# Kernel tuning notes

Hardware: AMD Instinct MI355X
Metric: run time of the kernel (lower is better)

## Reference

```python
import jax, jax.numpy as jnp
import numpy as np

B, S, D_MODEL, D_K, D_V, H = 2, 2048, 1024, 1024, 1024, 16


def setup_inputs() -> dict:
    key = jax.random.key(0)
    ks = jax.random.split(key, 12)
    s = 0.02
    inp = {
        "queries": jax.random.normal(ks[0], (B, S, D_MODEL), jnp.float32),
        "keys": jax.random.normal(ks[1], (B, S, D_MODEL), jnp.float32),
        "values": jax.random.normal(ks[2], (B, S, D_MODEL), jnp.float32),
        # causal mask: 1 where attention is disallowed (added as -1e9*mask)
        "mask": jnp.triu(jnp.ones((1, 1, S, S), jnp.float32), k=1),
        "Wq": jax.random.normal(ks[3], (D_MODEL, D_K), jnp.float32) * s,
        "bq": jnp.zeros((D_K,), jnp.float32),
        "Wk": jax.random.normal(ks[4], (D_MODEL, D_K), jnp.float32) * s,
        "bk": jnp.zeros((D_K,), jnp.float32),
        "Wv": jax.random.normal(ks[5], (D_MODEL, D_V), jnp.float32) * s,
        "bv": jnp.zeros((D_V,), jnp.float32),
        "Wo": jax.random.normal(ks[6], (D_K, D_MODEL), jnp.float32) * s,
        "bo": jnp.zeros((D_MODEL,), jnp.float32),
    }
    return inp


def _split_heads(x):  # [B,S,D] -> [B,H,S,D/H]
    b, s, d = x.shape
    return x.reshape(b, s, H, d // H).transpose(0, 2, 1, 3)


def reference(queries, keys, values, mask, Wq, bq, Wk, bk, Wv, bv, Wo, bo):
    q = _split_heads(queries @ Wq + bq)   # [B,H,S,hd]
    k = _split_heads(keys @ Wk + bk)
    v = _split_heads(values @ Wv + bv)
    # NOTE: original scales by sqrt(full d_k), not per-head dim (faithful quirk)
    scores = jnp.einsum("bhqd,bhkd->bhqk", q, k) / jnp.sqrt(jnp.float32(D_K))
    scores = scores + (-1e9) * mask
    w = jax.nn.softmax(scores, axis=-1)
    out = jnp.einsum("bhqk,bhkd->bhqd", w, v)        # [B,H,S,hd]
    out = out.transpose(0, 2, 1, 3).reshape(q.shape[0], q.shape[2], D_K)
    return out @ Wo + bo
```

## Files before the change

kernel.cpp:

```cpp
#include <hip/hip_runtime.h>
#include <hip/hip_bf16.h>
#include <cstdint>

typedef __bf16 bf16;
typedef __bf16 bf16x2 __attribute__((ext_vector_type(2)));
typedef __bf16 bf16x4 __attribute__((ext_vector_type(4)));
typedef __bf16 bf16x8 __attribute__((ext_vector_type(8)));
typedef float f32x4 __attribute__((ext_vector_type(4)));
typedef float f32x16 __attribute__((ext_vector_type(16)));
typedef unsigned int u32;

#define B_ 2
#define S_ 2048
#define DM 1024
#define H_ 16
#define HD 64

__device__ __forceinline__ void gload_lds16(const bf16* g, bf16* l) {
  __builtin_amdgcn_global_load_lds((const __attribute__((address_space(1))) void*)g,
                                   (__attribute__((address_space(3))) void*)l,
                                   16, 0, 0);
}

__device__ __forceinline__ u32 cvt_pk_bf16(float lo, float hi) {
  u32 r;
  asm("v_cvt_pk_bf16_f32 %0, %1, %2" : "=v"(r) : "v"(lo), "v"(hi));
  return r;
}

__global__ __launch_bounds__(256) void convert_k(const float* __restrict__ s0,
                                                 const float* __restrict__ s1,
                                                 const float* __restrict__ s2,
                                                 bf16* __restrict__ d0,
                                                 bf16* __restrict__ d1,
                                                 bf16* __restrict__ d2) {
  const float* s = (blockIdx.z == 0) ? s0 : (blockIdx.z == 1) ? s1 : s2;
  bf16* d = (blockIdx.z == 0) ? d0 : (blockIdx.z == 1) ? d1 : d2;
  const size_t i = ((size_t)blockIdx.x * 256 + threadIdx.x) * 8;
  f32x4 a = *(const f32x4*)(s + i);
  f32x4 b = *(const f32x4*)(s + i + 4);
  bf16x8 o;
#pragma unroll
  for (int j = 0; j < 4; j++) { o[j] = (bf16)a[j]; o[j + 4] = (bf16)b[j]; }
  *(bf16x8*)(d + i) = o;
}

__global__ __launch_bounds__(256) void transposeW_k(
    const float* __restrict__ w0, const float* __restrict__ w1,
    const float* __restrict__ w2, const float* __restrict__ w3,
    bf16* __restrict__ t0, bf16* __restrict__ t1,
    bf16* __restrict__ t2, bf16* __restrict__ t3) {
  const float* src = (blockIdx.z == 0) ? w0 : (blockIdx.z == 1) ? w1
                     : (blockIdx.z == 2) ? w2 : w3;
  bf16* dst = (blockIdx.z == 0) ? t0 : (blockIdx.z == 1) ? t1
              : (blockIdx.z == 2) ? t2 : t3;
  __shared__ float tile[32][33];
  const int tx = threadIdx.x, ty = threadIdx.y;
  const int x0 = blockIdx.x * 32, y0 = blockIdx.y * 32;
#pragma unroll
  for (int r = 0; r < 4; r++)
    tile[ty + r * 8][tx] = src[(size_t)(y0 + ty + r * 8) * DM + x0 + tx];
  __syncthreads();
#pragma unroll
  for (int r = 0; r < 4; r++)
    dst[(size_t)(x0 + ty + r * 8) * DM + y0 + tx] = (bf16)tile[tx][ty + r * 8];
}

struct GArgs { const void* A; const bf16* Bt; const float* bias; void* C; };
struct GArgs3 { GArgs g[3]; };

__global__ __launch_bounds__(512, 1) void gemm128_k(GArgs3 args, int M, int N,
                                                    int K) {
  __shared__ __align__(16) bf16 SA_[73728];
  bf16* const SB_ = SA_ + 24576;

  const int nwg = gridDim.x;
  const int id = blockIdx.x;
  const int wgid = (id & 7) * (nwg >> 3) + (id >> 3);
  const int z = wgid >> 7;
  const int rem = wgid & 127;
  const int tx = rem >> 5, ty = rem & 31;
  const GArgs ga = args.g[z];
  const int m0 = ty * 128, n0 = tx * 256;

  const int tid = threadIdx.x;
  const int lane = tid & 63, w = tid >> 6;
  const int l15 = lane & 15, q = lane >> 4;
  const int wr = w >> 2, wc = w & 3;

  const bf16* gA[2];
  const bf16* gB[4];
  int dA[2], dB[4];
#pragma unroll
  for (int i = 0; i < 2; i++) {
    const int ci = i * 512 + w * 64 + lane;
    const int row = ci >> 3, sc = (ci & 7) ^ (row & 7);
    gA[i] = (const bf16*)ga.A + (size_t)(m0 + row) * K + sc * 8;
    dA[i] = (i * 512 + w * 64) * 8;
  }
#pragma unroll
  for (int i = 0; i < 4; i++) {
    const int ci = i * 512 + w * 64 + lane;
    const int row = ci >> 3, sc = (ci & 7) ^ (row & 7);
    gB[i] = ga.Bt + (size_t)(n0 + row) * K + sc * 8;
    dB[i] = (i * 512 + w * 64) * 8;
  }

  const int cA0 = (q ^ (l15 & 7)) * 8;
  const int cA1 = ((4 + q) ^ (l15 & 7)) * 8;

  f32x4 acc[4][4] = {};

  const int NT = K >> 6;

#pragma unroll
  for (int tt = 0; tt < 2; tt++) {
    bf16* Ab = SA_ + tt * 8192;
    bf16* Bb = SB_ + tt * 16384;
    const int k0 = tt * 64;
    gload_lds16(gA[0] + k0, Ab + dA[0]);
    gload_lds16(gA[1] + k0, Ab + dA[1]);
#pragma unroll
    for (int i = 0; i < 4; i++) gload_lds16(gB[i] + k0, Bb + dB[i]);
  }
  asm volatile("s_waitcnt vmcnt(6)" ::: "memory");
  __builtin_amdgcn_s_barrier();

  for (int t = 0; t < NT; ++t) {
    const int rb = t % 3;
    const int wb = (t + 2) % 3;
    const int kpre = ((t + 2 < NT) ? t + 2 : NT - 1) << 6;
    {
      bf16* Ab = SA_ + wb * 8192;
      bf16* Bb = SB_ + wb * 16384;
      gload_lds16(gA[0] + kpre, Ab + dA[0]);
      gload_lds16(gA[1] + kpre, Ab + dA[1]);
#pragma unroll
      for (int i = 0; i < 4; i++) gload_lds16(gB[i] + kpre, Bb + dB[i]);
    }

    const bf16* Ab = SA_ + rb * 8192;
    const bf16* Bb = SB_ + rb * 16384;
    bf16x8 a[4][2], b[4][2];
#pragma unroll
    for (int mt = 0; mt < 4; mt++) {
      const int ro = (wr * 64 + mt * 16 + l15) * 64;
      a[mt][0] = *(const bf16x8*)(Ab + ro + cA0);
      a[mt][1] = *(const bf16x8*)(Ab + ro + cA1);
    }
#pragma unroll
    for (int nt = 0; nt < 4; nt++) {
      const int ro = (wc * 64 + nt * 16 + l15) * 64;
      b[nt][0] = *(const bf16x8*)(Bb + ro + cA0);
      b[nt][1] = *(const bf16x8*)(Bb + ro + cA1);
    }

    __builtin_amdgcn_s_setprio(1);
#pragma unroll
    for (int mt = 0; mt < 4; mt++)
#pragma unroll
      for (int nt = 0; nt < 4; nt++)
#pragma unroll
        for (int kk = 0; kk < 2; kk++)
          acc[mt][nt] = __builtin_amdgcn_mfma_f32_16x16x32_bf16(
              a[mt][kk], b[nt][kk], acc[mt][nt], 0, 0, 0);
    __builtin_amdgcn_s_setprio(0);

    asm volatile("s_waitcnt vmcnt(6)" ::: "memory");
    __builtin_amdgcn_s_barrier();
  }

  asm volatile("s_waitcnt vmcnt(0)" ::: "memory");
  __builtin_amdgcn_s_barrier();

  bf16* Ws = SA_ + w * 4352;
#pragma unroll
  for (int nt = 0; nt < 4; nt++) {
    const float bv = ga.bias[n0 + wc * 64 + nt * 16 + l15];
#pragma unroll
    for (int mt = 0; mt < 4; mt++)
#pragma unroll
      for (int r = 0; r < 4; r++)
        Ws[(mt * 16 + q * 4 + r) * 68 + nt * 16 + l15] =
            (bf16)(acc[mt][nt][r] + bv);
  }
#pragma unroll
  for (int p = 0; p < 8; p++) {
    const int lr = p * 8 + (lane >> 3), c0 = (lane & 7) * 8;
    bf16x4 lo = *(const bf16x4*)(Ws + lr * 68 + c0);
    bf16x4 hi = *(const bf16x4*)(Ws + lr * 68 + c0 + 4);
    bf16x8 o;
#pragma unroll
    for (int j = 0; j < 4; j++) { o[j] = lo[j]; o[j + 4] = hi[j]; }
    *(bf16x8*)((bf16*)ga.C + (size_t)(m0 + wr * 64 + lr) * N + n0 + wc * 64 + c0) = o;
  }
}

__global__ __launch_bounds__(512, 1) void gemmo_k(const bf16* __restrict__ A,
                                                  const bf16* __restrict__ Bt,
                                                  const float* __restrict__ bias,
                                                  float* __restrict__ C,
                                                  int M, int N, int K) {
  __shared__ __align__(16) bf16 SA_[49152];
  bf16* const SB_ = SA_ + 24576;

  const int id = blockIdx.x;
  const int wgid = (id & 7) * 32 + (id >> 3);
  const int tx = wgid >> 5, ty = wgid & 31;
  const int m0 = ty * 128, n0 = tx * 128;

  const int tid = threadIdx.x;
  const int lane = tid & 63, w = tid >> 6;
  const int l15 = lane & 15, q = lane >> 4;
  const int wr = w >> 2, wc = w & 3;

  const bf16* gA[2];
  const bf16* gB[2];
  int dd[2];
#pragma unroll
  for (int i = 0; i < 2; i++) {
    const int ci = i * 512 + w * 64 + lane;
    const int row = ci >> 3, sc = (ci & 7) ^ (row & 7);
    gA[i] = A + (size_t)(m0 + row) * K + sc * 8;
    gB[i] = Bt + (size_t)(n0 + row) * K + sc * 8;
    dd[i] = ci * 8;
  }

  const int cA0 = (q ^ (l15 & 7)) * 8;
  const int cA1 = ((4 + q) ^ (l15 & 7)) * 8;

  f32x4 acc[4][2] = {};
  const int NT = K >> 6;

#pragma unroll
  for (int tt = 0; tt < 2; tt++) {
    const int k0 = tt * 64;
    gload_lds16(gA[0] + k0, SA_ + tt * 8192 + dd[0]);
    gload_lds16(gA[1] + k0, SA_ + tt * 8192 + dd[1]);
    gload_lds16(gB[0] + k0, SB_ + tt * 8192 + dd[0]);
    gload_lds16(gB[1] + k0, SB_ + tt * 8192 + dd[1]);
  }
  asm volatile("s_waitcnt vmcnt(4)" ::: "memory");
  __builtin_amdgcn_s_barrier();

  for (int t = 0; t < NT; ++t) {
    const int rb = t % 3;
    const int wb = (t + 2) % 3;
    const int kpre = ((t + 2 < NT) ? t + 2 : NT - 1) << 6;
    gload_lds16(gA[0] + kpre, SA_ + wb * 8192 + dd[0]);
    gload_lds16(gA[1] + kpre, SA_ + wb * 8192 + dd[1]);
    gload_lds16(gB[0] + kpre, SB_ + wb * 8192 + dd[0]);
    gload_lds16(gB[1] + kpre, SB_ + wb * 8192 + dd[1]);

    const bf16* Ab = SA_ + rb * 8192;
    const bf16* Bb = SB_ + rb * 8192;
    bf16x8 a[4][2], b[2][2];
#pragma unroll
    for (int mt = 0; mt < 4; mt++) {
      const int ro = (wr * 64 + mt * 16 + l15) * 64;
      a[mt][0] = *(const bf16x8*)(Ab + ro + cA0);
      a[mt][1] = *(const bf16x8*)(Ab + ro + cA1);
    }
#pragma unroll
    for (int nt = 0; nt < 2; nt++) {
      const int ro = (wc * 32 + nt * 16 + l15) * 64;
      b[nt][0] = *(const bf16x8*)(Bb + ro + cA0);
      b[nt][1] = *(const bf16x8*)(Bb + ro + cA1);
    }

    __builtin_amdgcn_s_setprio(1);
#pragma unroll
    for (int mt = 0; mt < 4; mt++)
#pragma unroll
      for (int nt = 0; nt < 2; nt++)
#pragma unroll
        for (int kk = 0; kk < 2; kk++)
          acc[mt][nt] = __builtin_amdgcn_mfma_f32_16x16x32_bf16(
              a[mt][kk], b[nt][kk], acc[mt][nt], 0, 0, 0);
    __builtin_amdgcn_s_setprio(0);

    asm volatile("s_waitcnt vmcnt(4)" ::: "memory");
    __builtin_amdgcn_s_barrier();
  }

  asm volatile("s_waitcnt vmcnt(0)" ::: "memory");
  __builtin_amdgcn_s_barrier();

  float* Ws = (float*)SA_ + w * 2304;
#pragma unroll
  for (int nt = 0; nt < 2; nt++) {
    const float bv = bias[n0 + wc * 32 + nt * 16 + l15];
#pragma unroll
    for (int mt = 0; mt < 4; mt++)
#pragma unroll
      for (int r = 0; r < 4; r++)
        Ws[(mt * 16 + q * 4 + r) * 36 + nt * 16 + l15] = acc[mt][nt][r] + bv;
  }
#pragma unroll
  for (int p = 0; p < 8; p++) {
    const int lr = p * 8 + (lane >> 3), c0 = (lane & 7) * 4;
    f32x4 v = *(const f32x4*)(Ws + lr * 36 + c0);
    *(f32x4*)(C + (size_t)(m0 + wr * 64 + lr) * N + n0 + wc * 32 + c0) = v;
  }
}

template <bool AF32, bool CF32>
__global__ __launch_bounds__(256) void gemm_k(GArgs3 args, int M, int N, int K) {
  const GArgs ga = args.g[blockIdx.z];
  __shared__ __align__(16) bf16 As[128 * 32];
  __shared__ __align__(16) bf16 Bs[128 * 32];
  const int tid = threadIdx.x;
  const int lane = tid & 63, w = tid >> 6;
  const int l15 = lane & 15, q = lane >> 4;
  const int wr = w >> 1, wc = w & 1;
  const int m0 = blockIdx.y * 128, n0 = blockIdx.x * 128;

  const int c0 = w * 128 + lane;
  const int c1 = c0 + 64;
  const int r0 = c0 >> 2, r1 = c1 >> 2, koff = (c0 & 3) * 8;
  const bf16* gB0 = ga.Bt + (size_t)(n0 + r0) * K + koff;
  const bf16* gB1 = ga.Bt + (size_t)(n0 + r1) * K + koff;
  bf16* lA0 = As + (w * 2 + 0) * 512;
  bf16* lA1 = As + (w * 2 + 1) * 512;
  bf16* lB0 = Bs + (w * 2 + 0) * 512;
  bf16* lB1 = Bs + (w * 2 + 1) * 512;

  const float* pA0 = nullptr;
  const float* pA1 = nullptr;
  f32x4 t00, t01, t10, t11;
  if constexpr (AF32) {
    const float* A = (const float*)ga.A;
    pA0 = A + (size_t)(m0 + r0) * K + koff;
    pA1 = A + (size_t)(m0 + r1) * K + koff;
    t00 = *(const f32x4*)pA0; t01 = *(const f32x4*)(pA0 + 4);
    t10 = *(const f32x4*)pA1; t11 = *(const f32x4*)(pA1 + 4);
  }

  f32x4 acc[4][4] = {};

  for (int k0 = 0; k0 < K; k0 += 32) {
    if constexpr (AF32) {
      bf16x8 va0, va1;
#pragma unroll
      for (int j = 0; j < 4; j++) {
        va0[j] = (bf16)t00[j]; va0[j + 4] = (bf16)t01[j];
        va1[j] = (bf16)t10[j]; va1[j + 4] = (bf16)t11[j];
      }
      *(bf16x8*)(lA0 + lane * 8) = va0;
      *(bf16x8*)(lA1 + lane * 8) = va1;
    } else {
      const bf16* A = (const bf16*)ga.A;
      gload_lds16(A + (size_t)(m0 + r0) * K + koff + k0, lA0);
      gload_lds16(A + (size_t)(m0 + r1) * K + koff + k0, lA1);
    }
    gload_lds16(gB0 + k0, lB0);
    gload_lds16(gB1 + k0, lB1);
    __syncthreads();

    bf16x8 a[4], b[4];
#pragma unroll
    for (int mt = 0; mt < 4; mt++)
      a[mt] = *(const bf16x8*)(As + (wr * 64 + mt * 16 + l15) * 32 + q * 8);
#pragma unroll
    for (int nt = 0; nt < 4; nt++)
      b[nt] = *(const bf16x8*)(Bs + (wc * 64 + nt * 16 + l15) * 32 + q * 8);

    if constexpr (AF32) {
      const int kn = (k0 + 32 < K) ? k0 + 32 : k0;
      t00 = *(const f32x4*)(pA0 + kn); t01 = *(const f32x4*)(pA0 + kn + 4);
      t10 = *(const f32x4*)(pA1 + kn); t11 = *(const f32x4*)(pA1 + kn + 4);
    }

#pragma unroll
    for (int mt = 0; mt < 4; mt++)
#pragma unroll
      for (int nt = 0; nt < 4; nt++)
        acc[mt][nt] = __builtin_amdgcn_mfma_f32_16x16x32_bf16(a[mt], b[nt],
                                                              acc[mt][nt], 0, 0, 0);
    __syncthreads();
  }

#pragma unroll
  for (int nt = 0; nt < 4; nt++) {
    const int col = n0 + wc * 64 + nt * 16 + l15;
    const float bv = ga.bias[col];
#pragma unroll
    for (int mt = 0; mt < 4; mt++) {
      const int row = m0 + wr * 64 + mt * 16 + q * 4;
#pragma unroll
      for (int r = 0; r < 4; r++) {
        const float val = acc[mt][nt][r] + bv;
        if constexpr (CF32)
          ((float*)ga.C)[(size_t)(row + r) * N + col] = val;
        else
          ((bf16*)ga.C)[(size_t)(row + r) * N + col] = (bf16)val;
      }
    }
  }
}

__global__ __launch_bounds__(256, 4) void attn_k(const bf16* __restrict__ Qp,
                                                 const bf16* __restrict__ Kp,
                                                 const bf16* __restrict__ Vp,
                                                 bf16* __restrict__ Op) {
  const int g = blockIdx.x;
  const int xcd = g & 7, s = g >> 3;
  const int gl = s & 3, tau = s >> 2;
  const int bh = xcd * 4 + gl;
  const int b = bh >> 4, h = bh & 15;
  const int o3 = tau & 7, hq = tau >> 3;
  const int xt = (hq == 0) ? o3 : (hq == 1) ? 15 - o3
                 : (hq == 2) ? 16 + o3 : 31 - o3;
  const int i0 = xt * 64;

  const int tid = threadIdx.x;
  const int lane = tid & 63, w = tid >> 6;
  const int l31 = lane & 31, hi = lane >> 5;
  const int qh = w >> 1, kh = w & 1;

  __shared__ __align__(16) char smem[33280];
  bf16 (*Ks)[64][64] = (bf16 (*)[64][64])smem;
  bf16 (*Vts)[64][64] = (bf16 (*)[64][64])(smem + 16384);

  const size_t headoff = (size_t)b * S_ * DM + h * HD;
  const bf16* Kb = Kp + headoff;
  const bf16* Vb = Vp + headoff;

  const int kr0 = tid >> 3, kr1 = 32 + (tid >> 3), kcb = (tid & 7) * 8;
  const int cK = ((tid & 7) ^ (kr0 & 7)) * 8;
  const int d0 = (tid & 31) * 2, kq = (tid >> 5) * 8;
  const int cV0 = ((tid >> 5) ^ (d0 & 7)) * 8;
  const int cV1 = ((tid >> 5) ^ ((d0 + 1) & 7)) * 8;
  const float QSCALE = 0.04508422f;

  bf16x8 qreg[4];
  {
    const bf16* qb = Qp + headoff + (size_t)(i0 + qh * 32 + l31) * DM + hi * 8;
#pragma unroll
    for (int kk = 0; kk < 4; kk++) {
      bf16x8 v = *(const bf16x8*)(qb + kk * 16);
      bf16x8 o;
#pragma unroll
      for (int j = 0; j < 8; j++) o[j] = (bf16)((float)v[j] * QSCALE);
      qreg[kk] = o;
    }
  }

  const int NI = (i0 >> 6) + 1;

  bf16x8 kR0 = *(const bf16x8*)(Kb + (size_t)kr0 * DM + kcb);
  bf16x8 kR1 = *(const bf16x8*)(Kb + (size_t)kr1 * DM + kcb);
  bf16x2 vR[8];
#pragma unroll
  for (int j = 0; j < 8; j++)
    vR[j] = *(const bf16x2*)(Vb + (size_t)(kq + j) * DM + d0);
  *(bf16x8*)&Ks[0][kr0][cK] = kR0;
  *(bf16x8*)&Ks[0][kr1][cK] = kR1;
  {
    bf16x8 vlo, vhi;
#pragma unroll
    for (int j = 0; j < 8; j++) { vlo[j] = vR[j][0]; vhi[j] = vR[j][1]; }
    *(bf16x8*)&Vts[0][d0][cV0] = vlo;
    *(bf16x8*)&Vts[0][d0 + 1][cV1] = vhi;
  }
  if (NI > 1) {
    kR0 = *(const bf16x8*)(Kb + (size_t)(64 + kr0) * DM + kcb);
    kR1 = *(const bf16x8*)(Kb + (size_t)(64 + kr1) * DM + kcb);
#pragma unroll
    for (int j = 0; j < 8; j++)
      vR[j] = *(const bf16x2*)(Vb + (size_t)(64 + kq + j) * DM + d0);
  }
  __syncthreads();

  f32x16 oacc0 = {}, oacc1 = {};
  float rsum = 0.f;
  int buf = 0;

  for (int t = 0; t < NI; ++t, buf ^= 1) {
    if (t + 1 < NI) {
      *(bf16x8*)&Ks[buf ^ 1][kr0][cK] = kR0;
      *(bf16x8*)&Ks[buf ^ 1][kr1][cK] = kR1;
      bf16x8 vlo, vhi;
#pragma unroll
      for (int j = 0; j < 8; j++) { vlo[j] = vR[j][0]; vhi[j] = vR[j][1]; }
      *(bf16x8*)&Vts[buf ^ 1][d0][cV0] = vlo;
      *(bf16x8*)&Vts[buf ^ 1][d0 + 1][cV1] = vhi;
    }
    if (t + 2 < NI) {
      const size_t jn = (size_t)(t + 2) * 64;
      kR0 = *(const bf16x8*)(Kb + (jn + kr0) * DM + kcb);
      kR1 = *(const bf16x8*)(Kb + (jn + kr1) * DM + kcb);
#pragma unroll
      for (int j = 0; j < 8; j++)
        vR[j] = *(const bf16x2*)(Vb + (jn + kq + j) * DM + d0);
    }

    const bool diag = (t == NI - 1);
    if (!(diag && kh > qh)) {
      f32x16 sa = {}, sb = {};
      __builtin_amdgcn_s_setprio(1);
#pragma unroll
      for (int kk = 0; kk < 2; kk++) {
        bf16x8 ka = *(const bf16x8*)
            &Ks[buf][kh * 32 + l31][((2 * kk + hi) ^ (l31 & 7)) * 8];
        sa = __builtin_amdgcn_mfma_f32_32x32x16_bf16(ka, qreg[kk], sa, 0, 0, 0);
      }
#pragma unroll
      for (int kk = 2; kk < 4; kk++) {
        bf16x8 ka = *(const bf16x8*)
            &Ks[buf][kh * 32 + l31][((2 * kk + hi) ^ (l31 & 7)) * 8];
        sb = __builtin_amdgcn_mfma_f32_32x32x16_bf16(ka, qreg[kk], sb, 0, 0, 0);
      }
      __builtin_amdgcn_s_setprio(0);

      float p[16];
      if (diag) {
        const int qrl = qh * 32 + l31;
#pragma unroll
        for (int r = 0; r < 16; r++) {
          const int keyl = kh * 32 + (r & 3) + 8 * (r >> 2) + 4 * hi;
          p[r] = (keyl <= qrl) ? __builtin_amdgcn_exp2f(sa[r] + sb[r]) : 0.f;
        }
      } else {
#pragma unroll
        for (int r = 0; r < 16; r++)
          p[r] = __builtin_amdgcn_exp2f(sa[r] + sb[r]);
      }
      {
        float q0 = (p[0] + p[1]) + (p[2] + p[3]);
        float q1 = (p[4] + p[5]) + (p[6] + p[7]);
        float q2 = (p[8] + p[9]) + (p[10] + p[11]);
        float q3 = (p[12] + p[13]) + (p[14] + p[15]);
        rsum += (q0 + q1) + (q2 + q3);
      }

      u32 Aq[4][2];
#pragma unroll
      for (int t2 = 0; t2 < 4; t2++) {
        Aq[t2][0] = cvt_pk_bf16(p[4 * t2 + 0], p[4 * t2 + 1]);
        Aq[t2][1] = cvt_pk_bf16(p[4 * t2 + 2], p[4 * t2 + 3]);
      }
      bf16x8 pb[2];
#pragma unroll
      for (int s2 = 0; s2 < 2; s2++) {
        auto e0 = __builtin_amdgcn_permlane32_swap(Aq[2 * s2][0], Aq[2 * s2 + 1][0], false, false);
        auto e1 = __builtin_amdgcn_permlane32_swap(Aq[2 * s2][1], Aq[2 * s2 + 1][1], false, false);
        union { u32 u[4]; bf16x8 v; } cv;
        cv.u[0] = e0[0]; cv.u[1] = e1[0]; cv.u[2] = e0[1]; cv.u[3] = e1[1];
        pb[s2] = cv.v;
      }

      __builtin_amdgcn_s_setprio(1);
#pragma unroll
      for (int s2 = 0; s2 < 2; s2++) {
        const int cv = ((kh * 4 + s2 * 2 + hi) ^ (l31 & 7)) * 8;
        bf16x8 va0 = *(const bf16x8*)&Vts[buf][l31][cv];
        bf16x8 va1 = *(const bf16x8*)&Vts[buf][32 + l31][cv];
        oacc0 = __builtin_amdgcn_mfma_f32_32x32x16_bf16(va0, pb[s2], oacc0, 0, 0, 0);
        oacc1 = __builtin_amdgcn_mfma_f32_32x32x16_bf16(va1, pb[s2], oacc1, 0, 0, 0);
      }
      __builtin_amdgcn_s_setprio(0);
    }

    __syncthreads();
  }

  float rtot_w = rsum + __shfl_xor(rsum, 32);
  float* osum = (float*)smem;
  float* auxf = (float*)(smem + 32768);
#pragma unroll
  for (int m = 0; m < 2; m++) {
#pragma unroll
    for (int rq = 0; rq < 4; rq++) {
      f32x4 v4;
#pragma unroll
      for (int e = 0; e < 4; e++)
        v4[e] = m ? oacc1[rq * 4 + e] : oacc0[rq * 4 + e];
      *(f32x4*)(osum + w * 2048 + (m * 4 + rq) * 256 + lane * 4) = v4;
    }
  }
  if (lane < 32) auxf[w * 32 + lane] = rtot_w;
  __syncthreads();

  {
    const int q = tid >> 2, q31b = q & 31, qh2 = q >> 5;
    const float rtot = auxf[(qh2 * 2 + 0) * 32 + q31b] + auxf[(qh2 * 2 + 1) * 32 + q31b];
    const float rinv = 1.0f / rtot;
    const int dbase = (tid & 3) * 16;
    bf16* orow = Op + headoff + (size_t)(i0 + q) * DM + dbase;
#pragma unroll
    for (int gg = 0; gg < 2; gg++) {
      bf16x8 o8;
#pragma unroll
      for (int e = 0; e < 8; e++) {
        const int d = dbase + gg * 8 + e;
        const int base = (((d >> 5) << 2) | ((d >> 3) & 3)) * 256 +
                         (q31b + 32 * ((d >> 2) & 1)) * 4 + (d & 3);
        const float v = osum[(qh2 * 2 + 0) * 2048 + base] +
                        osum[(qh2 * 2 + 1) * 2048 + base];
        o8[e] = (bf16)(v * rinv);
      }
      *(bf16x8*)(orow + gg * 8) = o8;
    }
  }
}

extern "C" void kernel_launch(void* const* d_in, const int* in_sizes, int n_in,
                              void* d_out, int out_size, void* d_ws, size_t ws_size,
                              hipStream_t stream) {
  const float* q_in = (const float*)d_in[0];
  const float* k_in = (const float*)d_in[1];
  const float* v_in = (const float*)d_in[2];
  const float* Wq = (const float*)d_in[4];
  const float* bq = (const float*)d_in[5];
  const float* Wk = (const float*)d_in[6];
  const float* bk = (const float*)d_in[7];
  const float* Wv = (const float*)d_in[8];
  const float* bv = (const float*)d_in[9];
  const float* Wo = (const float*)d_in[10];
  const float* bo = (const float*)d_in[11];

  bf16* ws = (bf16*)d_ws;
  const size_t NQ = (size_t)B_ * S_ * DM;
  bf16* Qp = ws;
  bf16* Kp = ws + NQ;
  bf16* Vp = ws + 2 * NQ;
  bf16* WqT = ws + 3 * NQ;
  bf16* WkT = WqT + (size_t)DM * DM;
  bf16* WvT = WkT + (size_t)DM * DM;
  bf16* WoT = WvT + (size_t)DM * DM;
  bf16* qb = WoT + (size_t)DM * DM;
  bf16* kb = qb + NQ;
  bf16* vb = kb + NQ;

  const bool fast = ws_size >= (size_t)(28 * 1024 * 1024) * 2;

  transposeW_k<<<dim3(32, 32, 4), dim3(32, 8), 0, stream>>>(
      Wq, Wk, Wv, Wo, WqT, WkT, WvT, WoT);

  if (fast) {
    convert_k<<<dim3((B_ * S_ * DM) / (256 * 8), 1, 3), 256, 0, stream>>>(
        q_in, k_in, v_in, qb, kb, vb);
    GArgs3 g3;
    g3.g[0] = {qb, WqT, bq, Qp};
    g3.g[1] = {kb, WkT, bk, Kp};
    g3.g[2] = {vb, WvT, bv, Vp};
    gemm128_k<<<dim3(384), 512, 0, stream>>>(g3, B_ * S_, DM, DM);
  } else {
    GArgs3 g3;
    g3.g[0] = {q_in, WqT, bq, Qp};
    g3.g[1] = {k_in, WkT, bk, Kp};
    g3.g[2] = {v_in, WvT, bv, Vp};
    gemm_k<true, false><<<dim3(DM / 128, (B_ * S_) / 128, 3), 256, 0, stream>>>(
        g3, B_ * S_, DM, DM);
  }

  attn_k<<<dim3(1024, 1, 1), 256, 0, stream>>>(Qp, Kp, Vp, Qp);

  gemmo_k<<<dim3(256), 512, 0, stream>>>(Qp, WoT, bo, (float*)d_out,
                                         B_ * S_, DM, DM);
}
```

Baseline: 221.0 us.

## Enlarge attention query tile to 128 rows with 512-thread blocks

```diff
diff --git a/kernel.cpp b/kernel.cpp
--- a/kernel.cpp
+++ b/kernel.cpp
@@ -399,7 +399,7 @@
   }
 }
 
-__global__ __launch_bounds__(256, 4) void attn_k(const bf16* __restrict__ Qp,
+__global__ __launch_bounds__(512, 4) void attn_k(const bf16* __restrict__ Qp,
                                                  const bf16* __restrict__ Kp,
                                                  const bf16* __restrict__ Vp,
                                                  bf16* __restrict__ Op) {
@@ -408,17 +408,16 @@
   const int gl = s & 3, tau = s >> 2;
   const int bh = xcd * 4 + gl;
   const int b = bh >> 4, h = bh & 15;
-  const int o3 = tau & 7, hq = tau >> 3;
-  const int xt = (hq == 0) ? o3 : (hq == 1) ? 15 - o3
-                 : (hq == 2) ? 16 + o3 : 31 - o3;
-  const int i0 = xt * 64;
+  const int xt = (tau < 8) ? tau : 23 - tau;
+  const int i0 = xt * 128;
+  const int NI = 2 * xt + 2;
 
   const int tid = threadIdx.x;
   const int lane = tid & 63, w = tid >> 6;
   const int l31 = lane & 31, hi = lane >> 5;
-  const int qh = w >> 1, kh = w & 1;
-
-  __shared__ __align__(16) char smem[33280];
+  const int qq = w >> 1, kh = w & 1;
+
+  __shared__ __align__(16) char smem[33792];
   bf16 (*Ks)[64][64] = (bf16 (*)[64][64])smem;
   bf16 (*Vts)[64][64] = (bf16 (*)[64][64])(smem + 16384);
 
@@ -426,16 +425,16 @@
   const bf16* Kb = Kp + headoff;
   const bf16* Vb = Vp + headoff;
 
-  const int kr0 = tid >> 3, kr1 = 32 + (tid >> 3), kcb = (tid & 7) * 8;
-  const int cK = ((tid & 7) ^ (kr0 & 7)) * 8;
-  const int d0 = (tid & 31) * 2, kq = (tid >> 5) * 8;
-  const int cV0 = ((tid >> 5) ^ (d0 & 7)) * 8;
-  const int cV1 = ((tid >> 5) ^ ((d0 + 1) & 7)) * 8;
+  const int kr = tid >> 3, kcb = (tid & 7) * 8;
+  const int cK = ((tid & 7) ^ (kr & 7)) * 8;
+  const int d0 = (tid & 31) * 2, kq = (tid >> 5) * 4;
+  const int cV0 = ((kq >> 3) ^ (d0 & 7)) * 8 + (kq & 7);
+  const int cV1 = ((kq >> 3) ^ ((d0 + 1) & 7)) * 8 + (kq & 7);
   const float QSCALE = 0.04508422f;
 
   bf16x8 qreg[4];
   {
-    const bf16* qb = Qp + headoff + (size_t)(i0 + qh * 32 + l31) * DM + hi * 8;
+    const bf16* qb = Qp + headoff + (size_t)(i0 + qq * 32 + l31) * DM + hi * 8;
 #pragma unroll
     for (int kk = 0; kk < 4; kk++) {
       bf16x8 v = *(const bf16x8*)(qb + kk * 16);
@@ -446,57 +445,49 @@
     }
   }
 
-  const int NI = (i0 >> 6) + 1;
-
-  bf16x8 kR0 = *(const bf16x8*)(Kb + (size_t)kr0 * DM + kcb);
-  bf16x8 kR1 = *(const bf16x8*)(Kb + (size_t)kr1 * DM + kcb);
-  bf16x2 vR[8];
-#pragma unroll
-  for (int j = 0; j < 8; j++)
+  bf16x8 kR = *(const bf16x8*)(Kb + (size_t)kr * DM + kcb);
+  bf16x2 vR[4];
+#pragma unroll
+  for (int j = 0; j < 4; j++)
     vR[j] = *(const bf16x2*)(Vb + (size_t)(kq + j) * DM + d0);
-  *(bf16x8*)&Ks[0][kr0][cK] = kR0;
-  *(bf16x8*)&Ks[0][kr1][cK] = kR1;
+  *(bf16x8*)&Ks[0][kr][cK] = kR;
   {
-    bf16x8 vlo, vhi;
-#pragma unroll
-    for (int j = 0; j < 8; j++) { vlo[j] = vR[j][0]; vhi[j] = vR[j][1]; }
-    *(bf16x8*)&Vts[0][d0][cV0] = vlo;
-    *(bf16x8*)&Vts[0][d0 + 1][cV1] = vhi;
-  }
-  if (NI > 1) {
-    kR0 = *(const bf16x8*)(Kb + (size_t)(64 + kr0) * DM + kcb);
-    kR1 = *(const bf16x8*)(Kb + (size_t)(64 + kr1) * DM + kcb);
-#pragma unroll
-    for (int j = 0; j < 8; j++)
-      vR[j] = *(const bf16x2*)(Vb + (size_t)(64 + kq + j) * DM + d0);
-  }
+    bf16x4 vlo, vhi;
+#pragma unroll
+    for (int j = 0; j < 4; j++) { vlo[j] = vR[j][0]; vhi[j] = vR[j][1]; }
+    *(bf16x4*)&Vts[0][d0][cV0] = vlo;
+    *(bf16x4*)&Vts[0][d0 + 1][cV1] = vhi;
+  }
+  kR = *(const bf16x8*)(Kb + (size_t)(64 + kr) * DM + kcb);
+#pragma unroll
+  for (int j = 0; j < 4; j++)
+    vR[j] = *(const bf16x2*)(Vb + (size_t)(64 + kq + j) * DM + d0);
   __syncthreads();
 
   f32x16 oacc0 = {}, oacc1 = {};
   float rsum = 0.f;
   int buf = 0;
+  const int qbase = i0 + qq * 32;
 
   for (int t = 0; t < NI; ++t, buf ^= 1) {
     if (t + 1 < NI) {
-      *(bf16x8*)&Ks[buf ^ 1][kr0][cK] = kR0;
-      *(bf16x8*)&Ks[buf ^ 1][kr1][cK] = kR1;
-      bf16x8 vlo, vhi;
-#pragma unroll
-      for (int j = 0; j < 8; j++) { vlo[j] = vR[j][0]; vhi[j] = vR[j][1]; }
-      *(bf16x8*)&Vts[buf ^ 1][d0][cV0] = vlo;
-      *(bf16x8*)&Vts[buf ^ 1][d0 + 1][cV1] = vhi;
+      *(bf16x8*)&Ks[buf ^ 1][kr][cK] = kR;
+      bf16x4 vlo, vhi;
+#pragma unroll
+      for (int j = 0; j < 4; j++) { vlo[j] = vR[j][0]; vhi[j] = vR[j][1]; }
+      *(bf16x4*)&Vts[buf ^ 1][d0][cV0] = vlo;
+      *(bf16x4*)&Vts[buf ^ 1][d0 + 1][cV1] = vhi;
     }
     if (t + 2 < NI) {
       const size_t jn = (size_t)(t + 2) * 64;
-      kR0 = *(const bf16x8*)(Kb + (jn + kr0) * DM + kcb);
-      kR1 = *(const bf16x8*)(Kb + (jn + kr1) * DM + kcb);
-#pragma unroll
-      for (int j = 0; j < 8; j++)
+      kR = *(const bf16x8*)(Kb + (jn + kr) * DM + kcb);
+#pragma unroll
+      for (int j = 0; j < 4; j++)
         vR[j] = *(const bf16x2*)(Vb + (jn + kq + j) * DM + d0);
     }
 
-    const bool diag = (t == NI - 1);
-    if (!(diag && kh > qh)) {
+    const int kbase = t * 64 + kh * 32;
+    if (kbase <= qbase + 31) {
       f32x16 sa = {}, sb = {};
       __builtin_amdgcn_s_setprio(1);
 #pragma unroll
@@ -514,11 +505,11 @@
       __builtin_amdgcn_s_setprio(0);
 
       float p[16];
-      if (diag) {
-        const int qrl = qh * 32 + l31;
+      if (kbase + 31 > qbase) {
+        const int qrl = qbase + l31;
 #pragma unroll
         for (int r = 0; r < 16; r++) {
-          const int keyl = kh * 32 + (r & 3) + 8 * (r >> 2) + 4 * hi;
+          const int keyl = kbase + (r & 3) + 8 * (r >> 2) + 4 * hi;
           p[r] = (keyl <= qrl) ? __builtin_amdgcn_exp2f(sa[r] + sb[r]) : 0.f;
         }
       } else {
@@ -568,23 +559,38 @@
   float rtot_w = rsum + __shfl_xor(rsum, 32);
   float* osum = (float*)smem;
   float* auxf = (float*)(smem + 32768);
-#pragma unroll
-  for (int m = 0; m < 2; m++) {
-#pragma unroll
-    for (int rq = 0; rq < 4; rq++) {
-      f32x4 v4;
-#pragma unroll
-      for (int e = 0; e < 4; e++)
-        v4[e] = m ? oacc1[rq * 4 + e] : oacc0[rq * 4 + e];
-      *(f32x4*)(osum + w * 2048 + (m * 4 + rq) * 256 + lane * 4) = v4;
-    }
+  if (kh == 0) {
+#pragma unroll
+    for (int m = 0; m < 2; m++)
+#pragma unroll
+      for (int rq = 0; rq < 4; rq++) {
+        f32x4 v4;
+#pragma unroll
+        for (int e = 0; e < 4; e++)
+          v4[e] = m ? oacc1[rq * 4 + e] : oacc0[rq * 4 + e];
+        *(f32x4*)(osum + qq * 2048 + (m * 4 + rq) * 256 + lane * 4) = v4;
+      }
   }
   if (lane < 32) auxf[w * 32 + lane] = rtot_w;
   __syncthreads();
+  if (kh == 1) {
+#pragma unroll
+    for (int m = 0; m < 2; m++)
+#pragma unroll
+      for (int rq = 0; rq < 4; rq++) {
+        float* pp = osum + qq * 2048 + (m * 4 + rq) * 256 + lane * 4;
+        f32x4 v4 = *(f32x4*)pp;
+#pragma unroll
+        for (int e = 0; e < 4; e++)
+          v4[e] += m ? oacc1[rq * 4 + e] : oacc0[rq * 4 + e];
+        *(f32x4*)pp = v4;
+      }
+  }
+  __syncthreads();
 
   {
-    const int q = tid >> 2, q31b = q & 31, qh2 = q >> 5;
-    const float rtot = auxf[(qh2 * 2 + 0) * 32 + q31b] + auxf[(qh2 * 2 + 1) * 32 + q31b];
+    const int q = tid >> 2, q31b = q & 31, qq2 = q >> 5;
+    const float rtot = auxf[(qq2 * 2 + 0) * 32 + q31b] + auxf[(qq2 * 2 + 1) * 32 + q31b];
     const float rinv = 1.0f / rtot;
     const int dbase = (tid & 3) * 16;
     bf16* orow = Op + headoff + (size_t)(i0 + q) * DM + dbase;
@@ -596,9 +602,7 @@
         const int d = dbase + gg * 8 + e;
         const int base = (((d >> 5) << 2) | ((d >> 3) & 3)) * 256 +
                          (q31b + 32 * ((d >> 2) & 1)) * 4 + (d & 3);
-        const float v = osum[(qh2 * 2 + 0) * 2048 + base] +
-                        osum[(qh2 * 2 + 1) * 2048 + base];
-        o8[e] = (bf16)(v * rinv);
+        o8[e] = (bf16)(osum[qq2 * 2048 + base] * rinv);
       }
       *(bf16x8*)(orow + gg * 8) = o8;
     }
@@ -655,7 +659,7 @@
         g3, B_ * S_, DM, DM);
   }
 
-  attn_k<<<dim3(1024, 1, 1), 256, 0, stream>>>(Qp, Kp, Vp, Qp);
+  attn_k<<<dim3(512, 1, 1), 512, 0, stream>>>(Qp, Kp, Vp, Qp);
 
   gemmo_k<<<dim3(256), 512, 0, stream>>>(Qp, WoT, bo, (float*)d_out,
                                          B_ * S_, DM, DM);
```

Result: faster. 216.6 us (-2.0%).
